# Kernel tuning notes

Hardware: AMD Instinct MI355X
Metric: run time of the kernel (lower is better)

The kernel has to match this reference:

```python
import jax, jax.numpy as jnp
import numpy as np

N, F_IN, H, MH = 50000, 128, 128, 256
E = 800000

def _lin_init(key, out_d, in_d, bias=True):
    k1, k2 = jax.random.split(key)
    bound = 1.0 / np.sqrt(in_d)
    W = jax.random.uniform(k1, (out_d, in_d), minval=-bound, maxval=bound, dtype=jnp.float32)
    if bias:
        b = jax.random.uniform(k2, (out_d,), minval=-bound, maxval=bound, dtype=jnp.float32)
        return W, b
    return W, None

def setup_inputs() -> dict:
    key = jax.random.key(0)
    ks = jax.random.split(key, 8)
    x = jax.random.normal(ks[0], (N, F_IN), dtype=jnp.float32)
    edge_index = jax.random.randint(ks[1], (2, E), 0, N, dtype=jnp.int64)
    W1l, b1l = _lin_init(ks[2], H, F_IN, bias=True)   # SAGEConv1 neighbor lin (with bias)
    W1r, _ = _lin_init(ks[3], H, F_IN, bias=False)    # SAGEConv1 root lin (no bias)
    W2l, b2l = _lin_init(ks[4], H, H, bias=True)
    W2r, _ = _lin_init(ks[5], H, H, bias=False)
    Wm1, bm1 = _lin_init(ks[6], MH, 2 * H, bias=True)
    Wm2, bm2 = _lin_init(ks[7], 1, MH, bias=True)
    return {"x": x, "edge_index": edge_index,
            "W1l": W1l, "b1l": b1l, "W1r": W1r,
            "W2l": W2l, "b2l": b2l, "W2r": W2r,
            "Wm1": Wm1, "bm1": bm1, "Wm2": Wm2, "bm2": bm2}

def _sage_conv(x, src, dst, Wl, bl, Wr, num_nodes):
    # mean-aggregate messages x[src] at dst, then lin_l(agg) + lin_r(x)
    agg = jax.ops.segment_sum(x[src], dst, num_segments=num_nodes)
    cnt = jax.ops.segment_sum(jnp.ones((src.shape[0],), x.dtype), dst, num_segments=num_nodes)
    agg = agg / jnp.maximum(cnt, 1.0)[:, None]
    return agg @ Wl.T + bl + x @ Wr.T

def reference(x, edge_index, W1l, b1l, W1r, W2l, b2l, W2r, Wm1, bm1, Wm2, bm2):
    src, dst = edge_index[0], edge_index[1]
    n = x.shape[0]
    h = jax.nn.relu(_sage_conv(x, src, dst, W1l, b1l, W1r, n))
    # dropout is identity in eval mode
    h = jax.nn.relu(_sage_conv(h, src, dst, W2l, b2l, W2r, n))
    ef = jnp.concatenate([h[src], h[dst]], axis=-1)  # [E, 2H]
    out = jax.nn.relu(ef @ Wm1.T + bm1) @ Wm2.T + bm2
    return out.reshape(-1)
```

## Files before the change

kernel.cpp:

```cpp
#include <hip/hip_runtime.h>
#include <hip/hip_bf16.h>

#define NN 50000
#define F 128
#define EE 800000
#define MHD 256

typedef __attribute__((ext_vector_type(8))) short bf16x8;
typedef __attribute__((ext_vector_type(4))) float f32x4;

__device__ __forceinline__ float b2f(unsigned short u) {
    union { unsigned int i; float f; } v; v.i = ((unsigned)u) << 16; return v.f;
}
__device__ __forceinline__ unsigned short f2b(float f) {
    unsigned int x = __float_as_uint(f);
    unsigned int r = x + 0x7fffu + ((x >> 16) & 1u);
    return (unsigned short)(r >> 16);
}

__global__ __launch_bounds__(256) void cast_x_kernel(
    const float* __restrict__ in, unsigned short* __restrict__ out) {
    int i = (blockIdx.x * 256 + threadIdx.x) * 4;
    float4 v = *(const float4*)(in + i);
    ushort4 o; o.x = f2b(v.x); o.y = f2b(v.y); o.z = f2b(v.z); o.w = f2b(v.w);
    *(ushort4*)(out + i) = o;
}

__global__ __launch_bounds__(256) void cast_w_kernel(
    const float* __restrict__ W1l, const float* __restrict__ W1r,
    const float* __restrict__ W2l, const float* __restrict__ W2r,
    const float* __restrict__ Wm1, unsigned short* __restrict__ wb) {
    int i = (blockIdx.x * 256 + threadIdx.x) * 4;
    unsigned short o[4];
    if (i < 32768) {
        const float* p = (i < 16384) ? (W1l + i) : (W1r + (i - 16384));
        float4 v = *(const float4*)p;
        o[0] = f2b(v.x); o[1] = f2b(v.y); o[2] = f2b(v.z); o[3] = f2b(v.w);
    } else if (i < 65536) {
        int local = i - 32768;
        const float* M = (local < 16384) ? W2l : W2r;
        int lm = local & 16383;
        int n = lm >> 7, kp = lm & 127;
#pragma unroll
        for (int t = 0; t < 4; t++) {
            int k = ((kp + t) & 7) * 16 + ((kp + t) >> 3);
            o[t] = f2b(M[n * 128 + k]);
        }
    } else {
        int local = i - 65536;
        int n = local >> 8, k2 = local & 255;
        int half = k2 >> 7, kp = k2 & 127;
#pragma unroll
        for (int t = 0; t < 4; t++) {
            int k = half * 128 + ((kp + t) & 7) * 16 + ((kp + t) >> 3);
            o[t] = f2b(Wm1[n * 256 + k]);
        }
    }
    *(ushort4*)(wb + i) = *(ushort4*)o;
}

__global__ __launch_bounds__(256) void edge_cvt_hist_kernel(
    const int* __restrict__ ei, int* __restrict__ s32, int* __restrict__ d32,
    int* __restrict__ deg) {
    __shared__ int isI64;
    if (threadIdx.x == 0) {
        int z = 0;
        for (int i = 1; i < 128; i += 2) z |= ei[i];
        isI64 = (z == 0) ? 1 : 0;
    }
    __syncthreads();
    int e = blockIdx.x * 256 + threadIdx.x;
    if (e >= EE) return;
    int s, d;
    if (isI64) {
        const long long* e64 = (const long long*)ei;
        s = (int)e64[e];
        d = (int)e64[EE + e];
    } else {
        s = ei[e];
        d = ei[EE + e];
    }
    s32[e] = s;
    d32[e] = d;
    atomicAdd(&deg[d], 1);
}

__global__ __launch_bounds__(1024) void scan_p1_kernel(
    const int* __restrict__ deg, int* __restrict__ exloc, int* __restrict__ bsum) {
    __shared__ int part[1024];
    int t = threadIdx.x, gid = blockIdx.x * 1024 + t;
    int v = (gid < NN) ? deg[gid] : 0;
    part[t] = v;
    __syncthreads();
    for (int off = 1; off < 1024; off <<= 1) {
        int u = (t >= off) ? part[t - off] : 0;
        __syncthreads();
        part[t] += u;
        __syncthreads();
    }
    exloc[gid] = part[t] - v;
    if (t == 1023) bsum[blockIdx.x] = part[t];
}

__global__ __launch_bounds__(1024) void scan_p3_kernel(
    const int* __restrict__ exloc, const int* __restrict__ bsum,
    int* __restrict__ rowstart, int* __restrict__ cursor) {
    __shared__ int offs;
    if (threadIdx.x == 0) {
        int s = 0;
        for (int b = 0; b < blockIdx.x; b++) s += bsum[b];
        offs = s;
    }
    __syncthreads();
    int gid = blockIdx.x * 1024 + threadIdx.x;
    if (gid > NN) return;
    if (gid == NN) { rowstart[NN] = EE; return; }
    int r = exloc[gid] + offs;
    rowstart[gid] = r;
    cursor[gid] = r;
}

__global__ __launch_bounds__(256) void fill_kernel(
    const int* __restrict__ s32, const int* __restrict__ d32,
    int* __restrict__ cursor, int* __restrict__ nbr, int* __restrict__ eid) {
    int e = blockIdx.x * 256 + threadIdx.x;
    if (e < EE) {
        int p = atomicAdd(&cursor[d32[e]], 1);
        nbr[p] = s32[e];
        eid[p] = e;
    }
}

__global__ __launch_bounds__(256) void agg_gather_kernel(
    const unsigned short* __restrict__ xin,
    const int* __restrict__ nbr, const int* __restrict__ rowstart,
    unsigned short* __restrict__ aggb) {
    int wave = threadIdx.x >> 6, lane = threadIdx.x & 63;
    int node = blockIdx.x * 4 + wave;
    if (node >= NN) return;
    int part = lane >> 4;
    int col8 = (lane & 15) * 8;
    int beg = rowstart[node], end = rowstart[node + 1];
    float a[8] = {0,0,0,0,0,0,0,0};
    float b[8] = {0,0,0,0,0,0,0,0};
    int j = beg + part;
    for (; j + 12 < end; j += 16) {
        int s0 = nbr[j], s1 = nbr[j + 4], s2 = nbr[j + 8], s3 = nbr[j + 12];
        bf16x8 v0 = *(const bf16x8*)(xin + (size_t)s0 * F + col8);
        bf16x8 v1 = *(const bf16x8*)(xin + (size_t)s1 * F + col8);
        bf16x8 v2 = *(const bf16x8*)(xin + (size_t)s2 * F + col8);
        bf16x8 v3 = *(const bf16x8*)(xin + (size_t)s3 * F + col8);
        for (int i = 0; i < 8; i++) a[i] += b2f((unsigned short)v0[i]);
        for (int i = 0; i < 8; i++) b[i] += b2f((unsigned short)v1[i]);
        for (int i = 0; i < 8; i++) a[i] += b2f((unsigned short)v2[i]);
        for (int i = 0; i < 8; i++) b[i] += b2f((unsigned short)v3[i]);
    }
    for (; j + 4 < end; j += 8) {
        int s0 = nbr[j], s1 = nbr[j + 4];
        bf16x8 v0 = *(const bf16x8*)(xin + (size_t)s0 * F + col8);
        bf16x8 v1 = *(const bf16x8*)(xin + (size_t)s1 * F + col8);
        for (int i = 0; i < 8; i++) a[i] += b2f((unsigned short)v0[i]);
        for (int i = 0; i < 8; i++) b[i] += b2f((unsigned short)v1[i]);
    }
    if (j < end) {
        int s0 = nbr[j];
        bf16x8 v0 = *(const bf16x8*)(xin + (size_t)s0 * F + col8);
        for (int i = 0; i < 8; i++) a[i] += b2f((unsigned short)v0[i]);
    }
    float inv = 1.0f / fmaxf((float)(end - beg), 1.0f);
    unsigned short o[8];
    for (int i = 0; i < 8; i++) {
        float v = a[i] + b[i];
        v += __shfl_xor(v, 16);
        v += __shfl_xor(v, 32);
        o[i] = f2b(v * inv);
    }
    if (part == 0)
        *(bf16x8*)(aggb + (size_t)node * F + col8) = *(bf16x8*)o;
}

__global__ __launch_bounds__(256) void node_gemm_kernel(
    const unsigned short* __restrict__ A1, const unsigned short* __restrict__ A2,
    const unsigned short* __restrict__ W1, const unsigned short* __restrict__ W2,
    const float* __restrict__ bias,
    unsigned short* __restrict__ out) {
    int wave = threadIdx.x >> 6, lane = threadIdx.x & 63;
    int c = lane & 15, q = lane >> 4;
    int m0 = (blockIdx.x * 4 + wave) * 16;
    if (m0 >= NN) return;
    f32x4 acc[8];
    for (int nt = 0; nt < 8; nt++) {
        float b = bias[nt * 16 + c];
        acc[nt] = (f32x4){b, b, b, b};
    }
    int mrow = m0 + c; if (mrow > NN - 1) mrow = NN - 1;
    for (int op = 0; op < 2; op++) {
        const unsigned short* ap = (op ? A2 : A1) + (size_t)mrow * F + q * 8;
        const unsigned short* W  = op ? W2 : W1;
        for (int kb = 0; kb < 4; kb++) {
            bf16x8 a = *(const bf16x8*)(ap + kb * 32);
            for (int nt = 0; nt < 8; nt++) {
                bf16x8 b = *(const bf16x8*)(W + (size_t)(nt * 16 + c) * F + kb * 32 + q * 8);
                acc[nt] = __builtin_amdgcn_mfma_f32_16x16x32_bf16(a, b, acc[nt], 0, 0, 0);
            }
        }
    }
#pragma unroll
    for (int r = 0; r < 4; r++) {
        int node = m0 + q * 4 + r;
        if (node < NN) {
            unsigned short o[8];
#pragma unroll
            for (int nt = 0; nt < 8; nt++) o[nt] = f2b(fmaxf(acc[nt][r], 0.0f));
            *(bf16x8*)(out + (size_t)node * F + c * 8) = *(bf16x8*)o;
        }
    }
}

__global__ __launch_bounds__(256) void pq_gemm_kernel(
    const unsigned short* __restrict__ h,
    const unsigned short* __restrict__ wmb,
    const float* __restrict__ bm1,
    unsigned short* __restrict__ PQ) {
    int wave = threadIdx.x >> 6, lane = threadIdx.x & 63;
    int c = lane & 15, q = lane >> 4;
    int half = wave >> 1, ntBase = (wave & 1) * 8;
    int m0 = blockIdx.x * 16;
    int mrow = m0 + c; if (mrow > NN - 1) mrow = NN - 1;
    bf16x8 a[4];
#pragma unroll
    for (int kb = 0; kb < 4; kb++)
        a[kb] = *(const bf16x8*)(h + (size_t)mrow * F + kb * 32 + q * 8);
    f32x4 acc[8];
#pragma unroll
    for (int nt = 0; nt < 8; nt++) {
        float b = half ? bm1[(ntBase + nt) * 16 + c] : 0.0f;
        acc[nt] = (f32x4){b, b, b, b};
    }
#pragma unroll
    for (int kb = 0; kb < 4; kb++) {
#pragma unroll
        for (int nt = 0; nt < 8; nt++) {
            bf16x8 b = *(const bf16x8*)(wmb + (size_t)((ntBase + nt) * 16 + c) * 256 + half * 128 + kb * 32 + q * 8);
            acc[nt] = __builtin_amdgcn_mfma_f32_16x16x32_bf16(a[kb], b, acc[nt], 0, 0, 0);
        }
    }
#pragma unroll
    for (int r = 0; r < 4; r++) {
        int node = m0 + q * 4 + r;
        if (node < NN) {
            unsigned short o[8];
#pragma unroll
            for (int nt = 0; nt < 8; nt++) o[nt] = f2b(acc[nt][r]);
            *(bf16x8*)(PQ + (size_t)node * 512 + half * 256 + c * 16 + ntBase) = *(bf16x8*)o;
        }
    }
}

__global__ __launch_bounds__(256) void edge_dot_kernel(
    const unsigned short* __restrict__ PQ,
    const int* __restrict__ nbr, const int* __restrict__ eid,
    const int* __restrict__ rowstart,
    const float* __restrict__ Wm2, const float* __restrict__ bm2,
    float* __restrict__ out) {
    int wave = threadIdx.x >> 6, lane = threadIdx.x & 63;
    int node = blockIdx.x * 4 + wave;
    if (node >= NN) return;
    int g = lane >> 4, l16 = lane & 15;
    int col = l16 * 16;
    float w2f[16], qf[16];
#pragma unroll
    for (int i = 0; i < 16; i++) w2f[i] = Wm2[i * 16 + l16];
    {
        bf16x8 q0 = *(const bf16x8*)(PQ + (size_t)node * 512 + 256 + col);
        bf16x8 q1 = *(const bf16x8*)(PQ + (size_t)node * 512 + 256 + col + 8);
#pragma unroll
        for (int i = 0; i < 8; i++) { qf[i] = b2f((unsigned short)q0[i]); qf[8 + i] = b2f((unsigned short)q1[i]); }
    }
    float b2 = bm2[0];
    int beg = rowstart[node], end = rowstart[node + 1];
    int j = beg + g;
    for (; j + 4 < end; j += 8) {
        int s0 = nbr[j], s1 = nbr[j + 4];
        int id0 = eid[j], id1 = eid[j + 4];
        uint4 a0 = *(const uint4*)(PQ + (size_t)s0 * 512 + col);
        uint4 a1 = *(const uint4*)(PQ + (size_t)s0 * 512 + col + 8);
        uint4 c0 = *(const uint4*)(PQ + (size_t)s1 * 512 + col);
        uint4 c1 = *(const uint4*)(PQ + (size_t)s1 * 512 + col + 8);
        float t0 = 0.f, t1 = 0.f;
        unsigned int w0[8] = {a0.x, a0.y, a0.z, a0.w, a1.x, a1.y, a1.z, a1.w};
        unsigned int w1[8] = {c0.x, c0.y, c0.z, c0.w, c1.x, c1.y, c1.z, c1.w};
#pragma unroll
        for (int i = 0; i < 8; i++) {
            float lo0 = __uint_as_float(w0[i] << 16);
            float hi0 = __uint_as_float(w0[i] & 0xffff0000u);
            float lo1 = __uint_as_float(w1[i] << 16);
            float hi1 = __uint_as_float(w1[i] & 0xffff0000u);
            t0 += fmaxf(lo0 + qf[2 * i], 0.f) * w2f[2 * i]
                + fmaxf(hi0 + qf[2 * i + 1], 0.f) * w2f[2 * i + 1];
            t1 += fmaxf(lo1 + qf[2 * i], 0.f) * w2f[2 * i]
                + fmaxf(hi1 + qf[2 * i + 1], 0.f) * w2f[2 * i + 1];
        }
        t0 += __shfl_xor(t0, 1);  t1 += __shfl_xor(t1, 1);
        t0 += __shfl_xor(t0, 2);  t1 += __shfl_xor(t1, 2);
        t0 += __shfl_xor(t0, 4);  t1 += __shfl_xor(t1, 4);
        t0 += __shfl_xor(t0, 8);  t1 += __shfl_xor(t1, 8);
        if (l16 == 0) { out[id0] = t0 + b2; out[id1] = t1 + b2; }
    }
    for (; j < end; j += 4) {
        int s = nbr[j];
        int id = eid[j];
        uint4 a0 = *(const uint4*)(PQ + (size_t)s * 512 + col);
        uint4 a1 = *(const uint4*)(PQ + (size_t)s * 512 + col + 8);
        unsigned int w0[8] = {a0.x, a0.y, a0.z, a0.w, a1.x, a1.y, a1.z, a1.w};
        float t = 0.f;
#pragma unroll
        for (int i = 0; i < 8; i++) {
            float lo = __uint_as_float(w0[i] << 16);
            float hi = __uint_as_float(w0[i] & 0xffff0000u);
            t += fmaxf(lo + qf[2 * i], 0.f) * w2f[2 * i]
               + fmaxf(hi + qf[2 * i + 1], 0.f) * w2f[2 * i + 1];
        }
        t += __shfl_xor(t, 1);
        t += __shfl_xor(t, 2);
        t += __shfl_xor(t, 4);
        t += __shfl_xor(t, 8);
        if (l16 == 0) out[id] = t + b2;
    }
}

extern "C" void kernel_launch(void* const* d_in, const int* in_sizes, int n_in,
                              void* d_out, int out_size, void* d_ws, size_t ws_size,
                              hipStream_t stream) {
    const float* x   = (const float*)d_in[0];
    const int*   ei  = (const int*)d_in[1];
    const float* W1l = (const float*)d_in[2];
    const float* b1l = (const float*)d_in[3];
    const float* W1r = (const float*)d_in[4];
    const float* W2l = (const float*)d_in[5];
    const float* b2l = (const float*)d_in[6];
    const float* W2r = (const float*)d_in[7];
    const float* Wm1 = (const float*)d_in[8];
    const float* bm1 = (const float*)d_in[9];
    const float* Wm2 = (const float*)d_in[10];
    const float* bm2 = (const float*)d_in[11];

    char* ws = (char*)d_ws;
    unsigned short* PQ       = (unsigned short*)(ws);
    unsigned short* xb       = (unsigned short*)(ws);
    unsigned short* h1       = (unsigned short*)(ws + 12800000);
    unsigned short* aggb     = (unsigned short*)(ws + 25600000);
    unsigned short* wb       = (unsigned short*)(ws + 51200000);
    int*            s32      = (int*)(ws + 51462144);
    int*            d32      = (int*)(ws + 54662144);
    int*            deg      = (int*)(ws + 57862144);
    int*            rowstart = (int*)(ws + 58062208);
    int*            cursor   = (int*)(ws + 58262272);
    int*            nbr      = (int*)(ws + 58462336);
    int*            eid      = (int*)(ws + 61662336);
    unsigned short* h2       = (unsigned short*)(ws + 64862336);
    int*            exloc    = (int*)(ws + 77662336);
    int*            bsum     = (int*)(ws + 77867136);
    float*          outp     = (float*)d_out;

    const unsigned short* w1l_b  = wb;
    const unsigned short* w1r_b  = wb + 16384;
    const unsigned short* w2l_p  = wb + 32768;
    const unsigned short* w2r_p  = wb + 49152;
    const unsigned short* wm1_p  = wb + 65536;

    cast_x_kernel<<<6250, 256, 0, stream>>>(x, xb);
    cast_w_kernel<<<128, 256, 0, stream>>>(W1l, W1r, W2l, W2r, Wm1, wb);
    hipMemsetAsync(deg, 0, 200064, stream);
    edge_cvt_hist_kernel<<<3125, 256, 0, stream>>>(ei, s32, d32, deg);
    scan_p1_kernel<<<50, 1024, 0, stream>>>(deg, exloc, bsum);
    scan_p3_kernel<<<50, 1024, 0, stream>>>(exloc, bsum, rowstart, cursor);
    fill_kernel<<<3125, 256, 0, stream>>>(s32, d32, cursor, nbr, eid);

    agg_gather_kernel<<<12500, 256, 0, stream>>>(xb, nbr, rowstart, aggb);
    node_gemm_kernel<<<782, 256, 0, stream>>>(aggb, xb, w1l_b, w1r_b, b1l, h1);
    agg_gather_kernel<<<12500, 256, 0, stream>>>(h1, nbr, rowstart, aggb);
    node_gemm_kernel<<<782, 256, 0, stream>>>(aggb, h1, w2l_p, w2r_p, b2l, h2);
    pq_gemm_kernel<<<3125, 256, 0, stream>>>(h2, wm1_p, bm1, PQ);
    edge_dot_kernel<<<12500, 256, 0, stream>>>(PQ, nbr, eid, rowstart, Wm2, bm2, outp);
}
```

Measured before the change: 436.1 us.

## Fuse neighbor mean aggregation into SAGE node GEMM via LDS staging

```diff
diff --git a/kernel.cpp b/kernel.cpp
--- a/kernel.cpp
+++ b/kernel.cpp
@@ -131,63 +131,46 @@
     }
 }
 
-__global__ __launch_bounds__(256) void agg_gather_kernel(
+__global__ __launch_bounds__(256) void sage_layer_kernel(
     const unsigned short* __restrict__ xin,
     const int* __restrict__ nbr, const int* __restrict__ rowstart,
-    unsigned short* __restrict__ aggb) {
-    int wave = threadIdx.x >> 6, lane = threadIdx.x & 63;
-    int node = blockIdx.x * 4 + wave;
-    if (node >= NN) return;
-    int part = lane >> 4;
-    int col8 = (lane & 15) * 8;
-    int beg = rowstart[node], end = rowstart[node + 1];
-    float a[8] = {0,0,0,0,0,0,0,0};
-    float b[8] = {0,0,0,0,0,0,0,0};
-    int j = beg + part;
-    for (; j + 12 < end; j += 16) {
-        int s0 = nbr[j], s1 = nbr[j + 4], s2 = nbr[j + 8], s3 = nbr[j + 12];
-        bf16x8 v0 = *(const bf16x8*)(xin + (size_t)s0 * F + col8);
-        bf16x8 v1 = *(const bf16x8*)(xin + (size_t)s1 * F + col8);
-        bf16x8 v2 = *(const bf16x8*)(xin + (size_t)s2 * F + col8);
-        bf16x8 v3 = *(const bf16x8*)(xin + (size_t)s3 * F + col8);
-        for (int i = 0; i < 8; i++) a[i] += b2f((unsigned short)v0[i]);
-        for (int i = 0; i < 8; i++) b[i] += b2f((unsigned short)v1[i]);
-        for (int i = 0; i < 8; i++) a[i] += b2f((unsigned short)v2[i]);
-        for (int i = 0; i < 8; i++) b[i] += b2f((unsigned short)v3[i]);
-    }
-    for (; j + 4 < end; j += 8) {
-        int s0 = nbr[j], s1 = nbr[j + 4];
-        bf16x8 v0 = *(const bf16x8*)(xin + (size_t)s0 * F + col8);
-        bf16x8 v1 = *(const bf16x8*)(xin + (size_t)s1 * F + col8);
-        for (int i = 0; i < 8; i++) a[i] += b2f((unsigned short)v0[i]);
-        for (int i = 0; i < 8; i++) b[i] += b2f((unsigned short)v1[i]);
-    }
-    if (j < end) {
-        int s0 = nbr[j];
-        bf16x8 v0 = *(const bf16x8*)(xin + (size_t)s0 * F + col8);
-        for (int i = 0; i < 8; i++) a[i] += b2f((unsigned short)v0[i]);
-    }
-    float inv = 1.0f / fmaxf((float)(end - beg), 1.0f);
-    unsigned short o[8];
-    for (int i = 0; i < 8; i++) {
-        float v = a[i] + b[i];
-        v += __shfl_xor(v, 16);
-        v += __shfl_xor(v, 32);
-        o[i] = f2b(v * inv);
-    }
-    if (part == 0)
-        *(bf16x8*)(aggb + (size_t)node * F + col8) = *(bf16x8*)o;
-}
-
-__global__ __launch_bounds__(256) void node_gemm_kernel(
-    const unsigned short* __restrict__ A1, const unsigned short* __restrict__ A2,
     const unsigned short* __restrict__ W1, const unsigned short* __restrict__ W2,
     const float* __restrict__ bias,
     unsigned short* __restrict__ out) {
+    __shared__ unsigned short lds[4][16][136];
     int wave = threadIdx.x >> 6, lane = threadIdx.x & 63;
+    int m0 = (blockIdx.x * 4 + wave) * 16;
+
+    int g = lane >> 4, l16 = lane & 15, col8 = l16 * 8;
+    for (int batch = 0; batch < 4; batch++) {
+        int node = m0 + batch * 4 + g;
+        int beg = 0, end = 0;
+        if (node < NN) { beg = rowstart[node]; end = rowstart[node + 1]; }
+        float a[8] = {0,0,0,0,0,0,0,0};
+        int j = beg;
+        for (; j + 3 < end; j += 4) {
+            int s0 = nbr[j], s1 = nbr[j + 1], s2 = nbr[j + 2], s3 = nbr[j + 3];
+            bf16x8 v0 = *(const bf16x8*)(xin + (size_t)s0 * F + col8);
+            bf16x8 v1 = *(const bf16x8*)(xin + (size_t)s1 * F + col8);
+            bf16x8 v2 = *(const bf16x8*)(xin + (size_t)s2 * F + col8);
+            bf16x8 v3 = *(const bf16x8*)(xin + (size_t)s3 * F + col8);
+            for (int i = 0; i < 8; i++)
+                a[i] += (b2f((unsigned short)v0[i]) + b2f((unsigned short)v1[i]))
+                      + (b2f((unsigned short)v2[i]) + b2f((unsigned short)v3[i]));
+        }
+        for (; j < end; j++) {
+            int s0 = nbr[j];
+            bf16x8 v0 = *(const bf16x8*)(xin + (size_t)s0 * F + col8);
+            for (int i = 0; i < 8; i++) a[i] += b2f((unsigned short)v0[i]);
+        }
+        float inv = 1.0f / fmaxf((float)(end - beg), 1.0f);
+        unsigned short o[8];
+        for (int i = 0; i < 8; i++) o[i] = f2b(a[i] * inv);
+        *(bf16x8*)&lds[wave][batch * 4 + g][col8] = *(bf16x8*)o;
+    }
+    __syncthreads();
+
     int c = lane & 15, q = lane >> 4;
-    int m0 = (blockIdx.x * 4 + wave) * 16;
-    if (m0 >= NN) return;
     f32x4 acc[8];
     for (int nt = 0; nt < 8; nt++) {
         float b = bias[nt * 16 + c];
@@ -195,10 +178,11 @@
     }
     int mrow = m0 + c; if (mrow > NN - 1) mrow = NN - 1;
     for (int op = 0; op < 2; op++) {
-        const unsigned short* ap = (op ? A2 : A1) + (size_t)mrow * F + q * 8;
-        const unsigned short* W  = op ? W2 : W1;
+        const unsigned short* W = op ? W2 : W1;
         for (int kb = 0; kb < 4; kb++) {
-            bf16x8 a = *(const bf16x8*)(ap + kb * 32);
+            bf16x8 a;
+            if (op == 0) a = *(const bf16x8*)&lds[wave][c][kb * 32 + q * 8];
+            else         a = *(const bf16x8*)(xin + (size_t)mrow * F + kb * 32 + q * 8);
             for (int nt = 0; nt < 8; nt++) {
                 bf16x8 b = *(const bf16x8*)(W + (size_t)(nt * 16 + c) * F + kb * 32 + q * 8);
                 acc[nt] = __builtin_amdgcn_mfma_f32_16x16x32_bf16(a, b, acc[nt], 0, 0, 0);
@@ -349,7 +333,6 @@
     unsigned short* PQ       = (unsigned short*)(ws);
     unsigned short* xb       = (unsigned short*)(ws);
     unsigned short* h1       = (unsigned short*)(ws + 12800000);
-    unsigned short* aggb     = (unsigned short*)(ws + 25600000);
     unsigned short* wb       = (unsigned short*)(ws + 51200000);
     int*            s32      = (int*)(ws + 51462144);
     int*            d32      = (int*)(ws + 54662144);
@@ -377,10 +360,8 @@
     scan_p3_kernel<<<50, 1024, 0, stream>>>(exloc, bsum, rowstart, cursor);
     fill_kernel<<<3125, 256, 0, stream>>>(s32, d32, cursor, nbr, eid);
 
-    agg_gather_kernel<<<12500, 256, 0, stream>>>(xb, nbr, rowstart, aggb);
-    node_gemm_kernel<<<782, 256, 0, stream>>>(aggb, xb, w1l_b, w1r_b, b1l, h1);
-    agg_gather_kernel<<<12500, 256, 0, stream>>>(h1, nbr, rowstart, aggb);
-    node_gemm_kernel<<<782, 256, 0, stream>>>(aggb, h1, w2l_p, w2r_p, b2l, h2);
+    sage_layer_kernel<<<782, 256, 0, stream>>>(xb, nbr, rowstart, w1l_b, w1r_b, b1l, h1);
+    sage_layer_kernel<<<782, 256, 0, stream>>>(h1, nbr, rowstart, w2l_p, w2r_p, b2l, h2);
     pq_gemm_kernel<<<3125, 256, 0, stream>>>(h2, wm1_p, bm1, PQ);
     edge_dot_kernel<<<12500, 256, 0, stream>>>(PQ, nbr, eid, rowstart, Wm2, bm2, outp);
 }
```

Result: no change. 434.3 us (-0.4%).
